# Kernel optimization log

Hardware: AMD Instinct MI355X
Metric: run time of the kernel (lower is better)

The kernel has to match this reference:

```python
import jax, jax.numpy as jnp
import numpy as np
from jax import lax

L_MAX = 3          # n_ang_mom: l = 0, 1, 2
M_DIM = 2 * L_MAX - 1  # magnetic components, padded to 5
N_PAIRS = 40000
N_FEAT = 128


def hermite_features(g, n_features):
    """Orthonormal Hermite-function features h_0..h_{F-1}(g); [n] -> [n, F].

    Stable recurrence: h_{k+1} = sqrt(2/(k+1)) g h_k - sqrt(k/(k+1)) h_{k-1}.
    """
    h0 = (np.pi ** -0.25) * jnp.exp(-0.5 * g * g)
    h1 = jnp.sqrt(jnp.asarray(2.0, g.dtype)) * g * h0

    def step(carry, k):
        hkm1, hk = carry
        hkp1 = jnp.sqrt(2.0 / (k + 1.0)) * g * hk - jnp.sqrt(k / (k + 1.0)) * hkm1
        return (hk, hkp1), hkp1

    ks = jnp.arange(1, n_features - 1, dtype=g.dtype)  # produces h_2..h_{F-1}
    _, hs = lax.scan(step, (h0, h1), ks)
    feats = jnp.concatenate([h0[None], h1[None], hs], axis=0)  # [F, n]
    return feats.T  # [n, F]


def tensor_product(cg, a, b):
    """CG-style equivariant contraction.

    cg: [L, M, L, M, L, M] (sparse by selection rules), a, b: [L, M, n, F].
    out[l3, m3, n, f] = sum_{l1 m1 l2 m2} cg[l3,m3,l1,m1,l2,m2] a[l1,m1,n,f] b[l2,m2,n,f]
    """
    return jnp.einsum('lmabpq,abnf,pqnf->lmnf', cg, a, b)


def setup_inputs() -> dict:
    key = jax.random.key(0)
    k0, k1, k2, k3, k4 = jax.random.split(key, 5)
    L, M, N, F = L_MAX, M_DIM, N_PAIRS, N_FEAT
    x = jax.random.normal(k0, (L, M, N, F), dtype=jnp.float32)
    y = jax.random.normal(k1, (L, M, N, F), dtype=jnp.float32)
    g = jax.random.uniform(k2, (N,), dtype=jnp.float32, minval=0.5, maxval=5.0)
    scale = 1.0 / np.sqrt(F)  # GlorotNormal-like scaling
    w1 = jax.random.normal(k3, (F, F), dtype=jnp.float32) * scale
    w2 = jax.random.normal(k4, (F, F), dtype=jnp.float32) * scale
    # Clebsch-Gordan-like coefficient tensor with selection-rule sparsity:
    # nonzero only if |l1-l2| <= l3 <= l1+l2, |m_i| <= l_i, m3 == m1 + m2.
    rng = np.random.default_rng(0)
    cg = np.zeros((L, M, L, M, L, M), dtype=np.float32)
    c = L - 1  # m index offset: m -> m + c
    for l3 in range(L):
        for l1 in range(L):
            for l2 in range(L):
                if not (abs(l1 - l2) <= l3 <= l1 + l2):
                    continue
                for m1 in range(-l1, l1 + 1):
                    for m2 in range(-l2, l2 + 1):
                        m3 = m1 + m2
                        if abs(m3) <= l3:
                            cg[l3, m3 + c, l1, m1 + c, l2, m2 + c] = rng.standard_normal()
    return {"x": x, "y": y, "g": g, "w1": w1, "w2": w2, "cg": jnp.asarray(cg)}


def reference(x, y, g, w1, w2, cg):
    h = hermite_features(g, w1.shape[0])        # [n, F]
    w1g = jnp.einsum('fk,nk->nf', w1, h)        # [n, F]
    w2g = jnp.einsum('fk,nk->nf', w2, h)        # [n, F]
    a1 = w1g[None, None] * x                    # [L, M, n, F]
    b1 = w2g[None, None] * y
    a2 = w1g[None, None] * y
    b2 = w2g[None, None] * x
    res = tensor_product(cg, a1, b1) + tensor_product(cg, a2, b2)
    return res
```

## Files before the change

kernel.cpp:

```cpp
#include <hip/hip_runtime.h>
#include <array>

namespace {

constexpr int NPAIRS = 40000;
constexpr long NF = (long)NPAIRS * 128;

struct Term {
  int o, a, b;
};

constexpr int count_terms() {
  int idx = 0;
  for (int o = 0; o < 15; ++o) {
    const int l3 = o / 5, m3 = o % 5 - 2;
    if (m3 < -l3 || m3 > l3) continue;
    for (int l1 = 0; l1 < 3; ++l1)
      for (int l2 = 0; l2 < 3; ++l2) {
        const int ld = l1 > l2 ? l1 - l2 : l2 - l1;
        if (l3 < ld || l3 > l1 + l2) continue;
        const int mlo = (-l1 > m3 - l2) ? -l1 : m3 - l2;
        const int mhi = (l1 < m3 + l2) ? l1 : m3 + l2;
        for (int m1 = mlo; m1 <= mhi; ++m1) ++idx;
      }
  }
  return idx;
}
constexpr int NTERMS = count_terms();
static_assert(NTERMS == 117, "term count");

constexpr std::array<Term, NTERMS> make_terms() {
  std::array<Term, NTERMS> t{};
  int idx = 0;
  for (int o = 0; o < 15; ++o) {
    const int l3 = o / 5, m3 = o % 5 - 2;
    if (m3 < -l3 || m3 > l3) continue;
    for (int l1 = 0; l1 < 3; ++l1)
      for (int l2 = 0; l2 < 3; ++l2) {
        const int ld = l1 > l2 ? l1 - l2 : l2 - l1;
        if (l3 < ld || l3 > l1 + l2) continue;
        const int mlo = (-l1 > m3 - l2) ? -l1 : m3 - l2;
        const int mhi = (l1 < m3 + l2) ? l1 : m3 + l2;
        for (int m1 = mlo; m1 <= mhi; ++m1) {
          t[idx].o = o;
          t[idx].a = l1 * 5 + m1 + 2;
          t[idx].b = l2 * 5 + (m3 - m1) + 2;
          ++idx;
        }
      }
  }
  return t;
}
constexpr auto TERMS = make_terms();

constexpr std::array<int, 15> make_acc_idx() {
  std::array<int, 15> m{};
  for (int o = 0; o < 15; ++o) m[o] = -1;
  int q = 0;
  for (int o = 0; o < 15; ++o) {
    const int l3 = o / 5, m3 = o % 5 - 2;
    if (m3 >= -l3 && m3 <= l3) m[o] = q++;
  }
  return m;
}
constexpr auto ACC_IDX = make_acc_idx();

constexpr std::array<int, 9> make_used() {
  std::array<int, 9> u{};
  int q = 0;
  for (int o = 0; o < 15; ++o)
    if (ACC_IDX[o] >= 0) u[q++] = o;
  return u;
}
constexpr auto USED = make_used();

__constant__ constexpr int ZPLANES[6] = {0, 1, 3, 4, 5, 9};

__global__ __launch_bounds__(256, 4) void s_kernel(const float* __restrict__ g,
                                                   const float* __restrict__ w1,
                                                   const float* __restrict__ w2,
                                                   float* __restrict__ s_out,
                                                   float* __restrict__ out,
                                                   int zstart) {
  __shared__ float ht[128][32];
  __shared__ float wt1[16][132];
  __shared__ float wt2[16][132];

  const int tid = threadIdx.x;
  const int blk = blockIdx.x;

  if (tid < 32) {
    const float gv = g[blk * 32 + tid];
    float hkm1 = 0.75112554446494248286f * expf(-0.5f * gv * gv);
    float hk = 1.41421356237309504880f * gv * hkm1;
    ht[0][tid] = hkm1;
    ht[1][tid] = hk;
#pragma unroll 1
    for (int k = 1; k <= 126; ++k) {
      const float kf = (float)k;
      const float hkp1 =
          sqrtf(2.0f / (kf + 1.0f)) * gv * hk - sqrtf(kf / (kf + 1.0f)) * hkm1;
      ht[k + 1][tid] = hkp1;
      hkm1 = hk;
      hk = hkp1;
    }
  }

  {
    const long idx = (long)blk * 256 + tid;
    const float4 z = make_float4(0.f, 0.f, 0.f, 0.f);
    for (int zp = zstart; zp < 6; ++zp) {
      float* base = out + (long)ZPLANES[zp] * NF;
#pragma unroll
      for (int r = 0; r < 4; ++r)
        *(float4*)(base + (r * 320000 + idx) * 4) = z;
    }
  }

  const int fg = tid & 31;
  const int ng = tid >> 5;

  float acc1[4][4];
  float acc2[4][4];
#pragma unroll
  for (int i = 0; i < 4; ++i)
#pragma unroll
    for (int j = 0; j < 4; ++j) {
      acc1[i][j] = 0.f;
      acc2[i][j] = 0.f;
    }

  for (int kc = 0; kc < 8; ++kc) {
#pragma unroll
    for (int it = 0; it < 2; ++it) {
      const int lin = tid + it * 256;
      const int f = lin >> 2;
      const int kq = lin & 3;
      const float4 v1 = *(const float4*)(w1 + f * 128 + kc * 16 + kq * 4);
      const float4 v2 = *(const float4*)(w2 + f * 128 + kc * 16 + kq * 4);
      wt1[kq * 4 + 0][f] = v1.x;
      wt1[kq * 4 + 1][f] = v1.y;
      wt1[kq * 4 + 2][f] = v1.z;
      wt1[kq * 4 + 3][f] = v1.w;
      wt2[kq * 4 + 0][f] = v2.x;
      wt2[kq * 4 + 1][f] = v2.y;
      wt2[kq * 4 + 2][f] = v2.z;
      wt2[kq * 4 + 3][f] = v2.w;
    }
    __syncthreads();

#pragma unroll
    for (int kk = 0; kk < 16; ++kk) {
      const float4 wv1 = *(const float4*)&wt1[kk][fg * 4];
      const float4 wv2 = *(const float4*)&wt2[kk][fg * 4];
      const float4 ha = *(const float4*)&ht[kc * 16 + kk][ng * 4];
      const float hv[4] = {ha.x, ha.y, ha.z, ha.w};
#pragma unroll
      for (int i = 0; i < 4; ++i) {
        acc1[i][0] = fmaf(hv[i], wv1.x, acc1[i][0]);
        acc1[i][1] = fmaf(hv[i], wv1.y, acc1[i][1]);
        acc1[i][2] = fmaf(hv[i], wv1.z, acc1[i][2]);
        acc1[i][3] = fmaf(hv[i], wv1.w, acc1[i][3]);
        acc2[i][0] = fmaf(hv[i], wv2.x, acc2[i][0]);
        acc2[i][1] = fmaf(hv[i], wv2.y, acc2[i][1]);
        acc2[i][2] = fmaf(hv[i], wv2.z, acc2[i][2]);
        acc2[i][3] = fmaf(hv[i], wv2.w, acc2[i][3]);
      }
    }
    __syncthreads();
  }

#pragma unroll
  for (int i = 0; i < 4; ++i) {
    const long n = (long)blk * 32 + ng * 4 + i;
    float4 sv;
    sv.x = acc1[i][0] * acc2[i][0];
    sv.y = acc1[i][1] * acc2[i][1];
    sv.z = acc1[i][2] * acc2[i][2];
    sv.w = acc1[i][3] * acc2[i][3];
    *(float4*)(s_out + n * 128 + fg * 4) = sv;
  }
}

__global__ __launch_bounds__(256) void tp_kernel(const float* __restrict__ x,
                                                 const float* __restrict__ y,
                                                 const float* __restrict__ cg,
                                                 const float* __restrict__ s_in,
                                                 float* __restrict__ out,
                                                 int zero_p0) {
  __shared__ float d2s[NTERMS];
  const int tid = threadIdx.x;
  if (tid < NTERMS) {
    const Term tm = TERMS[tid];
    d2s[tid] = cg[(tm.o * 15 + tm.a) * 15 + tm.b] + cg[(tm.o * 15 + tm.b) * 15 + tm.a];
  }
  __syncthreads();

  const long off = ((long)blockIdx.x * 256 + tid) * 2;

  float2 xv[9], yv[9];
#pragma unroll
  for (int q = 0; q < 9; ++q) xv[q] = *(const float2*)(x + (long)USED[q] * NF + off);
#pragma unroll
  for (int q = 0; q < 9; ++q) yv[q] = *(const float2*)(y + (long)USED[q] * NF + off);
  const float2 sv = *(const float2*)(s_in + off);

  float accx[9], accy[9];
#pragma unroll
  for (int q = 0; q < 9; ++q) {
    accx[q] = 0.f;
    accy[q] = 0.f;
  }

#pragma unroll
  for (int t = 0; t < NTERMS; ++t) {
    const int qo = ACC_IDX[TERMS[t].o];
    const int qa = ACC_IDX[TERMS[t].a];
    const int qb = ACC_IDX[TERMS[t].b];
    const float c = d2s[t];
    accx[qo] = fmaf(c, xv[qa].x * yv[qb].x, accx[qo]);
    accy[qo] = fmaf(c, xv[qa].y * yv[qb].y, accy[qo]);
  }

  if (zero_p0) {
    *(float2*)(out + off) = make_float2(0.f, 0.f);
  }

#pragma unroll
  for (int q = 0; q < 9; ++q) {
    float2 r;
    r.x = accx[q] * sv.x;
    r.y = accy[q] * sv.y;
    *(float2*)(out + (long)USED[q] * NF + off) = r;
  }
}

}

extern "C" void kernel_launch(void* const* d_in, const int* in_sizes, int n_in,
                              void* d_out, int out_size, void* d_ws, size_t ws_size,
                              hipStream_t stream) {
  const float* x = (const float*)d_in[0];
  const float* y = (const float*)d_in[1];
  const float* g = (const float*)d_in[2];
  const float* w1 = (const float*)d_in[3];
  const float* w2 = (const float*)d_in[4];
  const float* cg = (const float*)d_in[5];
  float* out = (float*)d_out;

  const size_t s_bytes = (size_t)NF * sizeof(float);
  const bool use_ws = ws_size >= s_bytes;
  float* s_buf = use_ws ? (float*)d_ws : out;

  s_kernel<<<1250, 256, 0, stream>>>(g, w1, w2, s_buf, out, use_ws ? 0 : 1);
  tp_kernel<<<10000, 256, 0, stream>>>(x, y, cg, s_buf, out, use_ws ? 0 : 1);
}
```

Before: 203.7 us.

## Fuse feature-weight kernel and tensor-product kernel through shared-memory s tile

Merges the two launches into one kernel: each block computes its 32x128 product tile of the weighted Hermite features, keeps it in shared memory, then runs the CG contraction over the same 4096 elements and writes the output, including the zero planes. This removes the global round trip of the intermediate s buffer (write plus read of about 20 MB) and one launch. In exchange only 1250 blocks do the memory-heavy contraction, each looping 8 times, and shared-memory use per block grows, which could reduce occupancy and latency hiding.

```diff
diff --git a/kernel.cpp b/kernel.cpp
--- a/kernel.cpp
+++ b/kernel.cpp
@@ -74,20 +74,28 @@
 }
 constexpr auto USED = make_used();
 
-__constant__ constexpr int ZPLANES[6] = {0, 1, 3, 4, 5, 9};
-
-__global__ __launch_bounds__(256, 4) void s_kernel(const float* __restrict__ g,
-                                                   const float* __restrict__ w1,
-                                                   const float* __restrict__ w2,
-                                                   float* __restrict__ s_out,
-                                                   float* __restrict__ out,
-                                                   int zstart) {
+constexpr int ZPLANES[6] = {0, 1, 3, 4, 5, 9};
+
+__global__ __launch_bounds__(256) void fused_kernel(const float* __restrict__ x,
+                                                    const float* __restrict__ y,
+                                                    const float* __restrict__ g,
+                                                    const float* __restrict__ w1,
+                                                    const float* __restrict__ w2,
+                                                    const float* __restrict__ cg,
+                                                    float* __restrict__ out) {
   __shared__ float ht[128][32];
   __shared__ float wt1[16][132];
   __shared__ float wt2[16][132];
+  __shared__ float s_tile[4096];
+  __shared__ float d2s[NTERMS];
 
   const int tid = threadIdx.x;
   const int blk = blockIdx.x;
+
+  if (tid < NTERMS) {
+    const Term tm = TERMS[tid];
+    d2s[tid] = cg[(tm.o * 15 + tm.a) * 15 + tm.b] + cg[(tm.o * 15 + tm.b) * 15 + tm.a];
+  }
 
   if (tid < 32) {
     const float gv = g[blk * 32 + tid];
@@ -106,17 +114,6 @@
     }
   }
 
-  {
-    const long idx = (long)blk * 256 + tid;
-    const float4 z = make_float4(0.f, 0.f, 0.f, 0.f);
-    for (int zp = zstart; zp < 6; ++zp) {
-      float* base = out + (long)ZPLANES[zp] * NF;
-#pragma unroll
-      for (int r = 0; r < 4; ++r)
-        *(float4*)(base + (r * 320000 + idx) * 4) = z;
-    }
-  }
-
   const int fg = tid & 31;
   const int ng = tid >> 5;
 
@@ -172,66 +169,56 @@
 
 #pragma unroll
   for (int i = 0; i < 4; ++i) {
-    const long n = (long)blk * 32 + ng * 4 + i;
     float4 sv;
     sv.x = acc1[i][0] * acc2[i][0];
     sv.y = acc1[i][1] * acc2[i][1];
     sv.z = acc1[i][2] * acc2[i][2];
     sv.w = acc1[i][3] * acc2[i][3];
-    *(float4*)(s_out + n * 128 + fg * 4) = sv;
-  }
-}
-
-__global__ __launch_bounds__(256) void tp_kernel(const float* __restrict__ x,
-                                                 const float* __restrict__ y,
-                                                 const float* __restrict__ cg,
-                                                 const float* __restrict__ s_in,
-                                                 float* __restrict__ out,
-                                                 int zero_p0) {
-  __shared__ float d2s[NTERMS];
-  const int tid = threadIdx.x;
-  if (tid < NTERMS) {
-    const Term tm = TERMS[tid];
-    d2s[tid] = cg[(tm.o * 15 + tm.a) * 15 + tm.b] + cg[(tm.o * 15 + tm.b) * 15 + tm.a];
+    *(float4*)&s_tile[(ng * 4 + i) * 128 + fg * 4] = sv;
   }
   __syncthreads();
 
-  const long off = ((long)blockIdx.x * 256 + tid) * 2;
-
-  float2 xv[9], yv[9];
-#pragma unroll
-  for (int q = 0; q < 9; ++q) xv[q] = *(const float2*)(x + (long)USED[q] * NF + off);
-#pragma unroll
-  for (int q = 0; q < 9; ++q) yv[q] = *(const float2*)(y + (long)USED[q] * NF + off);
-  const float2 sv = *(const float2*)(s_in + off);
-
-  float accx[9], accy[9];
-#pragma unroll
-  for (int q = 0; q < 9; ++q) {
-    accx[q] = 0.f;
-    accy[q] = 0.f;
-  }
-
-#pragma unroll
-  for (int t = 0; t < NTERMS; ++t) {
-    const int qo = ACC_IDX[TERMS[t].o];
-    const int qa = ACC_IDX[TERMS[t].a];
-    const int qb = ACC_IDX[TERMS[t].b];
-    const float c = d2s[t];
-    accx[qo] = fmaf(c, xv[qa].x * yv[qb].x, accx[qo]);
-    accy[qo] = fmaf(c, xv[qa].y * yv[qb].y, accy[qo]);
-  }
-
-  if (zero_p0) {
-    *(float2*)(out + off) = make_float2(0.f, 0.f);
-  }
-
-#pragma unroll
-  for (int q = 0; q < 9; ++q) {
-    float2 r;
-    r.x = accx[q] * sv.x;
-    r.y = accy[q] * sv.y;
-    *(float2*)(out + (long)USED[q] * NF + off) = r;
+  const long wbase = (long)blk * 4096;
+  for (int j = 0; j < 8; ++j) {
+    const int e = j * 512 + tid * 2;
+    const long off = wbase + e;
+
+#pragma unroll
+    for (int zp = 0; zp < 6; ++zp) {
+      *(float2*)(out + (long)ZPLANES[zp] * NF + off) = make_float2(0.f, 0.f);
+    }
+
+    float2 xv[9], yv[9];
+#pragma unroll
+    for (int q = 0; q < 9; ++q) xv[q] = *(const float2*)(x + (long)USED[q] * NF + off);
+#pragma unroll
+    for (int q = 0; q < 9; ++q) yv[q] = *(const float2*)(y + (long)USED[q] * NF + off);
+    const float2 sv = *(const float2*)&s_tile[e];
+
+    float accx[9], accy[9];
+#pragma unroll
+    for (int q = 0; q < 9; ++q) {
+      accx[q] = 0.f;
+      accy[q] = 0.f;
+    }
+
+#pragma unroll
+    for (int t = 0; t < NTERMS; ++t) {
+      const int qo = ACC_IDX[TERMS[t].o];
+      const int qa = ACC_IDX[TERMS[t].a];
+      const int qb = ACC_IDX[TERMS[t].b];
+      const float c = d2s[t];
+      accx[qo] = fmaf(c, xv[qa].x * yv[qb].x, accx[qo]);
+      accy[qo] = fmaf(c, xv[qa].y * yv[qb].y, accy[qo]);
+    }
+
+#pragma unroll
+    for (int q = 0; q < 9; ++q) {
+      float2 r;
+      r.x = accx[q] * sv.x;
+      r.y = accy[q] * sv.y;
+      *(float2*)(out + (long)USED[q] * NF + off) = r;
+    }
   }
 }
 
@@ -248,10 +235,5 @@
   const float* cg = (const float*)d_in[5];
   float* out = (float*)d_out;
 
-  const size_t s_bytes = (size_t)NF * sizeof(float);
-  const bool use_ws = ws_size >= s_bytes;
-  float* s_buf = use_ws ? (float*)d_ws : out;
-
-  s_kernel<<<1250, 256, 0, stream>>>(g, w1, w2, s_buf, out, use_ws ? 0 : 1);
-  tp_kernel<<<10000, 256, 0, stream>>>(x, y, cg, s_buf, out, use_ws ? 0 : 1);
-}
+  fused_kernel<<<1250, 256, 0, stream>>>(x, y, g, w1, w2, cg, out);
+}
```

Measured after the change: 496.2 us. 144% more time.
